# Performance work log

Hardware: AMD Instinct MI355X
Metric: run time of the kernel (lower is better)

## Reference

```python
import jax, jax.numpy as jnp
import numpy as np

IN_FEATURES = 4096
OUT_FEATURES = 4096
SHARED_ROWS = 512
BATCH = 4096


def setup_inputs() -> dict:
    key = jax.random.key(0)
    k1, k2, k3 = jax.random.split(key, 3)
    x = jax.random.normal(k1, (BATCH, IN_FEATURES), dtype=jnp.float32)
    shared_weights = jax.random.normal(k2, (SHARED_ROWS, IN_FEATURES), dtype=jnp.float32)
    bias = jax.random.normal(k3, (OUT_FEATURES,), dtype=jnp.float32)
    return {"x": x, "shared_weights": shared_weights, "bias": bias}


def reference(x, shared_weights, bias):
    # Original: W = shared_weights.repeat(out_features // shared_rows, 1)  -> [out, in]
    #           y = x @ W.T + bias
    # Row i of W equals shared_weights[i % shared_rows], so the output columns are a
    # tile of the small GEMM result — compute the small GEMM once and tile (same math,
    # avoids materializing the full [out, in] weight).
    reps = OUT_FEATURES // SHARED_ROWS
    y_small = jnp.einsum("bi,ri->br", x, shared_weights)  # [batch, shared_rows]
    y = jnp.tile(y_small, (1, reps)) + bias  # [batch, out_features]
    return y
```

## Files before the change

### kernel.cpp

```cpp
#include <hip/hip_runtime.h>
#include <hip/hip_bf16.h>


typedef __bf16 bf8 __attribute__((ext_vector_type(8)));
typedef float f4 __attribute__((ext_vector_type(4)));
typedef unsigned int uint;

constexpr int M = 4096;
constexpr int K = 4096;
constexpr int NS = 512;
constexpr int OUTF = 4096;
constexpr int BM = 128, BN = 128, BK = 32;
constexpr int SK = 8;
constexpr int KS = K / SK;
constexpr int BKP = BK + 8;

#define PERM_HI2(hi, lo) __builtin_amdgcn_perm((hi), (lo), 0x07060302u)

__global__ __launch_bounds__(256, 3)
void gemm_split_kernel(const float* __restrict__ x, const float* __restrict__ w,
                       float* __restrict__ out) {
  __shared__ __align__(16) unsigned short As[BM * BKP];
  __shared__ __align__(16) unsigned short Bs[BN * BKP];

  const int gid = blockIdx.x;
  const int mt = gid & 31;
  const int nt = (gid >> 5) & 3;
  const int s  = gid >> 7;

  const int tid = threadIdx.x;
  const int row2 = tid >> 1;
  const int kc   = (tid & 1) << 4;

  const float* xA = x + (size_t)(mt * BM + row2) * K + s * KS + kc;
  const float* wB = w + (size_t)(nt * BN + row2) * K + s * KS + kc;

  const int lane = tid & 63;
  const int wv = tid >> 6;
  const int wm = (wv & 1) * 64;
  const int wn = (wv >> 1) * 64;
  const int lr = lane & 15;
  const int lq = lane >> 4;

  f4 acc[4][4] = {};

  float4 ga[4], gb[4];
#pragma unroll
  for (int i = 0; i < 4; ++i) {
    ga[i] = *reinterpret_cast<const float4*>(xA + i * 4);
    gb[i] = *reinterpret_cast<const float4*>(wB + i * 4);
  }

  constexpr int NITER = KS / BK;
  for (int kk = 0; kk < NITER; ++kk) {
    uint4 u0 = __builtin_bit_cast(uint4, ga[0]);
    uint4 u1 = __builtin_bit_cast(uint4, ga[1]);
    uint4 u2 = __builtin_bit_cast(uint4, ga[2]);
    uint4 u3 = __builtin_bit_cast(uint4, ga[3]);
    uint4 pa0, pa1;
    pa0.x = PERM_HI2(u0.y, u0.x); pa0.y = PERM_HI2(u0.w, u0.z);
    pa0.z = PERM_HI2(u1.y, u1.x); pa0.w = PERM_HI2(u1.w, u1.z);
    pa1.x = PERM_HI2(u2.y, u2.x); pa1.y = PERM_HI2(u2.w, u2.z);
    pa1.z = PERM_HI2(u3.y, u3.x); pa1.w = PERM_HI2(u3.w, u3.z);
    *reinterpret_cast<uint4*>(&As[row2 * BKP + kc])     = pa0;
    *reinterpret_cast<uint4*>(&As[row2 * BKP + kc + 8]) = pa1;

    uint4 v0 = __builtin_bit_cast(uint4, gb[0]);
    uint4 v1 = __builtin_bit_cast(uint4, gb[1]);
    uint4 v2 = __builtin_bit_cast(uint4, gb[2]);
    uint4 v3 = __builtin_bit_cast(uint4, gb[3]);
    uint4 pb0, pb1;
    pb0.x = PERM_HI2(v0.y, v0.x); pb0.y = PERM_HI2(v0.w, v0.z);
    pb0.z = PERM_HI2(v1.y, v1.x); pb0.w = PERM_HI2(v1.w, v1.z);
    pb1.x = PERM_HI2(v2.y, v2.x); pb1.y = PERM_HI2(v2.w, v2.z);
    pb1.z = PERM_HI2(v3.y, v3.x); pb1.w = PERM_HI2(v3.w, v3.z);
    *reinterpret_cast<uint4*>(&Bs[row2 * BKP + kc])     = pb0;
    *reinterpret_cast<uint4*>(&Bs[row2 * BKP + kc + 8]) = pb1;

    __syncthreads();

    if (kk + 1 < NITER) {
      const float* xn = xA + (kk + 1) * BK;
      const float* wn2 = wB + (kk + 1) * BK;
#pragma unroll
      for (int i = 0; i < 4; ++i) {
        ga[i] = *reinterpret_cast<const float4*>(xn + i * 4);
        gb[i] = *reinterpret_cast<const float4*>(wn2 + i * 4);
      }
    }

    bf8 af[4], bfv[4];
#pragma unroll
    for (int mf = 0; mf < 4; ++mf)
      af[mf] = *reinterpret_cast<const bf8*>(&As[(wm + mf * 16 + lr) * BKP + lq * 8]);
#pragma unroll
    for (int nf = 0; nf < 4; ++nf)
      bfv[nf] = *reinterpret_cast<const bf8*>(&Bs[(wn + nf * 16 + lr) * BKP + lq * 8]);

#pragma unroll
    for (int mf = 0; mf < 4; ++mf)
#pragma unroll
      for (int nf = 0; nf < 4; ++nf)
        acc[mf][nf] = __builtin_amdgcn_mfma_f32_16x16x32_bf16(af[mf], bfv[nf], acc[mf][nf], 0, 0, 0);

    __syncthreads();
  }

  float* ob = out + (size_t)(mt * BM) * OUTF + s * NS + nt * BN;
#pragma unroll
  for (int mf = 0; mf < 4; ++mf) {
#pragma unroll
    for (int nf = 0; nf < 4; ++nf) {
#pragma unroll
      for (int r = 0; r < 4; ++r) {
        const int row = wm + mf * 16 + lq * 4 + r;
        const int col = wn + nf * 16 + lr;
        ob[(size_t)row * OUTF + col] = acc[mf][nf][r];
      }
    }
  }
}

__global__ __launch_bounds__(256)
void combine_kernel(float* __restrict__ out, const float* __restrict__ bias) {
  const int t = blockIdx.x * 256 + threadIdx.x;
  const int b  = t >> 7;
  const int rc = t & 127;
  float4* row = reinterpret_cast<float4*>(out) + (size_t)b * (OUTF / 4);
  const float4* bias4 = reinterpret_cast<const float4*>(bias);

  float4 p[8];
#pragma unroll
  for (int s2 = 0; s2 < 8; ++s2) p[s2] = row[s2 * 128 + rc];

  float sx = 0.f, sy = 0.f, sz = 0.f, sw = 0.f;
#pragma unroll
  for (int s2 = 0; s2 < 8; ++s2) {
    sx += p[s2].x; sy += p[s2].y; sz += p[s2].z; sw += p[s2].w;
  }

#pragma unroll
  for (int s2 = 0; s2 < 8; ++s2) {
    float4 bb = bias4[s2 * 128 + rc];
    float4 o;
    o.x = sx + bb.x; o.y = sy + bb.y; o.z = sz + bb.z; o.w = sw + bb.w;
    row[s2 * 128 + rc] = o;
  }
}

extern "C" void kernel_launch(void* const* d_in, const int* in_sizes, int n_in,
                              void* d_out, int out_size, void* d_ws, size_t ws_size,
                              hipStream_t stream) {
  (void)in_sizes; (void)n_in; (void)d_ws; (void)ws_size; (void)out_size;
  const float* x    = (const float*)d_in[0];
  const float* w    = (const float*)d_in[1];
  const float* bias = (const float*)d_in[2];
  float* out = (float*)d_out;

  gemm_split_kernel<<<dim3(32 * 4 * SK), dim3(256), 0, stream>>>(x, w, out);
  combine_kernel<<<dim3((M * NS / 4) / 256), dim3(256), 0, stream>>>(out, bias);
}
```

Measured before the change: 185.9 us.

## Double-buffer LDS tiles with two-stage register prefetch and halve split-K

Adds double-buffered shared-memory tiles and a two-deep global-load prefetch so the next tile is packed to LDS after the MFMAs and only one barrier is needed per iteration. Split-K drops from 8 to 4, which halves the partial-sum traffic through the output buffer in the combine kernel but also halves the grid to 512 blocks. The occupancy hint is lowered to 2 blocks per CU to allow for the extra registers and LDS. Fewer blocks may underfill the GPU's compute units.

```diff
diff --git a/kernel.cpp b/kernel.cpp
--- a/kernel.cpp
+++ b/kernel.cpp
@@ -11,17 +11,29 @@
 constexpr int NS = 512;
 constexpr int OUTF = 4096;
 constexpr int BM = 128, BN = 128, BK = 32;
-constexpr int SK = 8;
+constexpr int SK = 4;
 constexpr int KS = K / SK;
+constexpr int NITER = KS / BK;
 constexpr int BKP = BK + 8;
 
 #define PERM_HI2(hi, lo) __builtin_amdgcn_perm((hi), (lo), 0x07060302u)
 
-__global__ __launch_bounds__(256, 3)
+__device__ __forceinline__ void pack_tile(const float4 g[4], uint4& p0, uint4& p1) {
+  uint4 u0 = __builtin_bit_cast(uint4, g[0]);
+  uint4 u1 = __builtin_bit_cast(uint4, g[1]);
+  uint4 u2 = __builtin_bit_cast(uint4, g[2]);
+  uint4 u3 = __builtin_bit_cast(uint4, g[3]);
+  p0.x = PERM_HI2(u0.y, u0.x); p0.y = PERM_HI2(u0.w, u0.z);
+  p0.z = PERM_HI2(u1.y, u1.x); p0.w = PERM_HI2(u1.w, u1.z);
+  p1.x = PERM_HI2(u2.y, u2.x); p1.y = PERM_HI2(u2.w, u2.z);
+  p1.z = PERM_HI2(u3.y, u3.x); p1.w = PERM_HI2(u3.w, u3.z);
+}
+
+__global__ __launch_bounds__(256, 2)
 void gemm_split_kernel(const float* __restrict__ x, const float* __restrict__ w,
                        float* __restrict__ out) {
-  __shared__ __align__(16) unsigned short As[BM * BKP];
-  __shared__ __align__(16) unsigned short Bs[BN * BKP];
+  __shared__ __align__(16) unsigned short As[2][BM * BKP];
+  __shared__ __align__(16) unsigned short Bs[2][BN * BKP];
 
   const int gid = blockIdx.x;
   const int mt = gid & 31;
@@ -44,58 +56,47 @@
 
   f4 acc[4][4] = {};
 
-  float4 ga[4], gb[4];
+  float4 ga[2][4], gb[2][4];
 #pragma unroll
   for (int i = 0; i < 4; ++i) {
-    ga[i] = *reinterpret_cast<const float4*>(xA + i * 4);
-    gb[i] = *reinterpret_cast<const float4*>(wB + i * 4);
+    ga[0][i] = *reinterpret_cast<const float4*>(xA + i * 4);
+    gb[0][i] = *reinterpret_cast<const float4*>(wB + i * 4);
+    ga[1][i] = *reinterpret_cast<const float4*>(xA + BK + i * 4);
+    gb[1][i] = *reinterpret_cast<const float4*>(wB + BK + i * 4);
   }
 
-  constexpr int NITER = KS / BK;
+  {
+    uint4 p0, p1;
+    pack_tile(ga[0], p0, p1);
+    *reinterpret_cast<uint4*>(&As[0][row2 * BKP + kc])     = p0;
+    *reinterpret_cast<uint4*>(&As[0][row2 * BKP + kc + 8]) = p1;
+    pack_tile(gb[0], p0, p1);
+    *reinterpret_cast<uint4*>(&Bs[0][row2 * BKP + kc])     = p0;
+    *reinterpret_cast<uint4*>(&Bs[0][row2 * BKP + kc + 8]) = p1;
+  }
+  __syncthreads();
+
   for (int kk = 0; kk < NITER; ++kk) {
-    uint4 u0 = __builtin_bit_cast(uint4, ga[0]);
-    uint4 u1 = __builtin_bit_cast(uint4, ga[1]);
-    uint4 u2 = __builtin_bit_cast(uint4, ga[2]);
-    uint4 u3 = __builtin_bit_cast(uint4, ga[3]);
-    uint4 pa0, pa1;
-    pa0.x = PERM_HI2(u0.y, u0.x); pa0.y = PERM_HI2(u0.w, u0.z);
-    pa0.z = PERM_HI2(u1.y, u1.x); pa0.w = PERM_HI2(u1.w, u1.z);
-    pa1.x = PERM_HI2(u2.y, u2.x); pa1.y = PERM_HI2(u2.w, u2.z);
-    pa1.z = PERM_HI2(u3.y, u3.x); pa1.w = PERM_HI2(u3.w, u3.z);
-    *reinterpret_cast<uint4*>(&As[row2 * BKP + kc])     = pa0;
-    *reinterpret_cast<uint4*>(&As[row2 * BKP + kc + 8]) = pa1;
-
-    uint4 v0 = __builtin_bit_cast(uint4, gb[0]);
-    uint4 v1 = __builtin_bit_cast(uint4, gb[1]);
-    uint4 v2 = __builtin_bit_cast(uint4, gb[2]);
-    uint4 v3 = __builtin_bit_cast(uint4, gb[3]);
-    uint4 pb0, pb1;
-    pb0.x = PERM_HI2(v0.y, v0.x); pb0.y = PERM_HI2(v0.w, v0.z);
-    pb0.z = PERM_HI2(v1.y, v1.x); pb0.w = PERM_HI2(v1.w, v1.z);
-    pb1.x = PERM_HI2(v2.y, v2.x); pb1.y = PERM_HI2(v2.w, v2.z);
-    pb1.z = PERM_HI2(v3.y, v3.x); pb1.w = PERM_HI2(v3.w, v3.z);
-    *reinterpret_cast<uint4*>(&Bs[row2 * BKP + kc])     = pb0;
-    *reinterpret_cast<uint4*>(&Bs[row2 * BKP + kc + 8]) = pb1;
-
-    __syncthreads();
-
-    if (kk + 1 < NITER) {
-      const float* xn = xA + (kk + 1) * BK;
-      const float* wn2 = wB + (kk + 1) * BK;
-#pragma unroll
-      for (int i = 0; i < 4; ++i) {
-        ga[i] = *reinterpret_cast<const float4*>(xn + i * 4);
-        gb[i] = *reinterpret_cast<const float4*>(wn2 + i * 4);
-      }
-    }
+    const int cur = kk & 1;
+    const int nxt = cur ^ 1;
 
     bf8 af[4], bfv[4];
 #pragma unroll
     for (int mf = 0; mf < 4; ++mf)
-      af[mf] = *reinterpret_cast<const bf8*>(&As[(wm + mf * 16 + lr) * BKP + lq * 8]);
+      af[mf] = *reinterpret_cast<const bf8*>(&As[cur][(wm + mf * 16 + lr) * BKP + lq * 8]);
 #pragma unroll
     for (int nf = 0; nf < 4; ++nf)
-      bfv[nf] = *reinterpret_cast<const bf8*>(&Bs[(wn + nf * 16 + lr) * BKP + lq * 8]);
+      bfv[nf] = *reinterpret_cast<const bf8*>(&Bs[cur][(wn + nf * 16 + lr) * BKP + lq * 8]);
+
+    if (kk + 2 < NITER) {
+      const float* xn = xA + (kk + 2) * BK;
+      const float* wn2 = wB + (kk + 2) * BK;
+#pragma unroll
+      for (int i = 0; i < 4; ++i) {
+        ga[cur][i] = *reinterpret_cast<const float4*>(xn + i * 4);
+        gb[cur][i] = *reinterpret_cast<const float4*>(wn2 + i * 4);
+      }
+    }
 
 #pragma unroll
     for (int mf = 0; mf < 4; ++mf)
@@ -103,6 +104,15 @@
       for (int nf = 0; nf < 4; ++nf)
         acc[mf][nf] = __builtin_amdgcn_mfma_f32_16x16x32_bf16(af[mf], bfv[nf], acc[mf][nf], 0, 0, 0);
 
+    if (kk + 1 < NITER) {
+      uint4 p0, p1;
+      pack_tile(ga[nxt], p0, p1);
+      *reinterpret_cast<uint4*>(&As[nxt][row2 * BKP + kc])     = p0;
+      *reinterpret_cast<uint4*>(&As[nxt][row2 * BKP + kc + 8]) = p1;
+      pack_tile(gb[nxt], p0, p1);
+      *reinterpret_cast<uint4*>(&Bs[nxt][row2 * BKP + kc])     = p0;
+      *reinterpret_cast<uint4*>(&Bs[nxt][row2 * BKP + kc + 8]) = p1;
+    }
     __syncthreads();
   }
 
@@ -129,22 +139,22 @@
   float4* row = reinterpret_cast<float4*>(out) + (size_t)b * (OUTF / 4);
   const float4* bias4 = reinterpret_cast<const float4*>(bias);
 
-  float4 p[8];
+  float4 p[SK];
 #pragma unroll
-  for (int s2 = 0; s2 < 8; ++s2) p[s2] = row[s2 * 128 + rc];
+  for (int s2 = 0; s2 < SK; ++s2) p[s2] = row[s2 * 128 + rc];
 
   float sx = 0.f, sy = 0.f, sz = 0.f, sw = 0.f;
 #pragma unroll
-  for (int s2 = 0; s2 < 8; ++s2) {
+  for (int s2 = 0; s2 < SK; ++s2) {
     sx += p[s2].x; sy += p[s2].y; sz += p[s2].z; sw += p[s2].w;
   }
 
 #pragma unroll
-  for (int s2 = 0; s2 < 8; ++s2) {
-    float4 bb = bias4[s2 * 128 + rc];
+  for (int c = 0; c < 8; ++c) {
+    float4 bb = bias4[c * 128 + rc];
     float4 o;
     o.x = sx + bb.x; o.y = sy + bb.y; o.z = sz + bb.z; o.w = sw + bb.w;
-    row[s2 * 128 + rc] = o;
+    row[c * 128 + rc] = o;
   }
 }
 
```

Measured after the change: 316.7 us. +70.4%, slower.
